# Kernel tuning notes

Hardware: AMD Instinct MI355X
Metric: run time of the kernel (lower is better)

The kernel has to match this reference:

```python
import jax, jax.numpy as jnp
import numpy as np

B, C, N, F = 256, 4, 64, 256   # batch, in_channels, neighbors, in_features
OC, OF = 8, 256                # out_channels, out_features


def setup_inputs() -> dict:
    key = jax.random.key(0)
    k1, k2, k3, k4, k5 = jax.random.split(key, 5)
    x = jax.random.normal(k1, (B, C, F), dtype=jnp.float32)
    neighbor = jax.random.normal(k2, (B, N, C, F), dtype=jnp.float32)
    # torch.nn.Linear weights are (out_features, in_features)
    W_att1 = jax.random.normal(k3, (C, F), dtype=jnp.float32) / np.sqrt(F).astype(np.float32)
    W_att2 = jax.random.normal(k4, (C, F), dtype=jnp.float32) / np.sqrt(F).astype(np.float32)
    # Conv1d weight: (out_c*out_f, 2C, F); kernel_size==F makes it a dense contraction
    W_conv = jax.random.normal(k5, (OC * OF, 2 * C, F), dtype=jnp.float32) / np.sqrt(2 * C * F).astype(np.float32)
    return {"x": x, "neighbor": neighbor, "W_att1": W_att1, "W_att2": W_att2, "W_conv": W_conv}


def reference(x, neighbor, W_att1, W_att2, W_conv):
    # --- attention weights: einsum 'ci,nkl->n' = sum(att1(x_i)) * sum_{k,l} att2(y_i)[n]
    s1 = jnp.sum(x @ W_att1.T, axis=(1, 2))              # (B,)
    s2 = jnp.sum(neighbor @ W_att2.T, axis=(2, 3))       # (B, N)
    w = jax.nn.softmax(s1[:, None] * s2, axis=1)         # softmax over neighbors (dim 0 per-sample)

    # --- feature adjacency: einsum 'ca,ncb,n->cab' vectorized over batch
    fadj = jnp.einsum('bcx,bncy,bn->bcxy', x, neighbor, w)   # (B, C, F, F)
    fadj = fadj + jnp.swapaxes(fadj, -1, -2)
    # sgnroot
    fadj = jnp.sign(fadj) * jnp.sqrt(jnp.clip(jnp.abs(fadj), 1e-8, None))
    # row normalize over dim -2, NaN -> 0
    adj = fadj / (jnp.abs(fadj).sum(axis=-2, keepdims=True) + 1e-7)
    adj = jnp.where(jnp.isnan(adj), jnp.float32(0.0), adj)

    # --- transform: cat([adj @ x, x], channel) then full-width conv1d (dense contraction)
    h = jnp.einsum('bcxy,bcy->bcx', adj, x)              # (B, C, F)
    z = jnp.concatenate([h, x], axis=1)                  # (B, 2C, F)
    out = jnp.einsum('bcf,ocf->bo', z, W_conv).reshape(B, OC, OF)
    return out, adj
```

## Files before the change

### kernel.cpp

```cpp
#include <hip/hip_runtime.h>
#include <hip/hip_bf16.h>
#include <math.h>


typedef __bf16 bf16x8 __attribute__((ext_vector_type(8)));
typedef __bf16 bf16x4 __attribute__((ext_vector_type(4)));
typedef float f32x4 __attribute__((ext_vector_type(4)));

#define NB 256
#define NC 4
#define NN 64
#define NF 256
#define NO 2048

__global__ __launch_bounds__(256) void k_pre(
    const float* __restrict__ x, const float* __restrict__ nb,
    const float* __restrict__ W1, const float* __restrict__ W2,
    const float* __restrict__ Wc,
    __hip_bfloat16* __restrict__ Wcb, __hip_bfloat16* __restrict__ zbf,
    float* __restrict__ s1, float* __restrict__ s2)
{
  __shared__ float red[4];
  int t = threadIdx.x;
  int gid = blockIdx.x;

  if (gid < 16640) {
    int fi = t & 63;
    const float4* Wf4 = (const float4*)((gid < 16384) ? W2 : W1);
    float4 w0 = Wf4[fi], w1 = Wf4[64 + fi], w2 = Wf4[128 + fi], w3 = Wf4[192 + fi];
    float4 wv = { w0.x + w1.x + w2.x + w3.x,
                  w0.y + w1.y + w2.y + w3.y,
                  w0.z + w1.z + w2.z + w3.z,
                  w0.w + w1.w + w2.w + w3.w };
    const float4* src = (gid < 16384) ? ((const float4*)nb + (size_t)gid * 256)
                                      : ((const float4*)x + (size_t)(gid - 16384) * 256);
    float4 nv = src[t];
    float val = fmaf(nv.x, wv.x, fmaf(nv.y, wv.y, fmaf(nv.z, wv.z, nv.w * wv.w)));
    for (int off = 32; off > 0; off >>= 1) val += __shfl_down(val, off);
    if ((t & 63) == 0) red[t >> 6] = val;
    __syncthreads();
    if (t == 0) {
      float s = red[0] + red[1] + red[2] + red[3];
      if (gid < 16384) s2[gid] = s;
      else s1[gid - 16384] = s;
    }
  } else if (gid < 20736) {
    int idx = (gid - 16640) * 256 + t;
    float4 v = ((const float4*)Wc)[idx];
    bf16x4 o = { (__bf16)v.x, (__bf16)v.y, (__bf16)v.z, (__bf16)v.w };
    ((bf16x4*)Wcb)[idx] = o;
  } else {
    int i = (gid - 20736) * 256 + t;
    int e = i * 4;
    int b = e >> 10, r = e & 1023;
    float4 v = ((const float4*)x)[i];
    bf16x4 o = { (__bf16)v.x, (__bf16)v.y, (__bf16)v.z, (__bf16)v.w };
    *(bf16x4*)(zbf + (size_t)b * 2048 + 1024 + r) = o;
  }
}

__global__ __launch_bounds__(256) void k_adj(
    const float* __restrict__ x, const float* __restrict__ nb,
    const float* __restrict__ s1, const float* __restrict__ s2,
    float* __restrict__ adj, __hip_bfloat16* __restrict__ zbf)
{
  __shared__ float xs[256], ns[256], invs[256], wsh[64];
  __shared__ float part[4][256];
  int t = threadIdx.x;
  int w = t >> 6, l = t & 63;
  int blk = blockIdx.x;
  int b = blk >> 2, c = blk & 3;

  if (t < 64) {
    float v = s1[b] * s2[b * 64 + t];
    float m = v;
    for (int off = 32; off > 0; off >>= 1) m = fmaxf(m, __shfl_xor(m, off));
    float e = expf(v - m);
    float s = e;
    for (int off = 32; off > 0; off >>= 1) s += __shfl_xor(s, off);
    wsh[t] = e / s;
  }
  xs[t] = x[(size_t)blk * 256 + t];
  __syncthreads();

  const float4* nb4 = (const float4*)(nb + (size_t)b * 65536 + c * 256);
  float4 a4 = {0.f, 0.f, 0.f, 0.f};
  #pragma unroll
  for (int k = 0; k < 16; ++k) {
    int n = w + 4 * k;
    float4 v = nb4[(size_t)n * 256 + l];
    float wn = wsh[n];
    a4.x = fmaf(wn, v.x, a4.x);
    a4.y = fmaf(wn, v.y, a4.y);
    a4.z = fmaf(wn, v.z, a4.z);
    a4.w = fmaf(wn, v.w, a4.w);
  }
  *(float4*)&part[w][l * 4] = a4;
  __syncthreads();
  ns[t] = part[0][t] + part[1][t] + part[2][t] + part[3][t];
  __syncthreads();

  int j0 = l * 4;
  float4 xv = *(const float4*)&xs[j0];
  float4 nv = *(const float4*)&ns[j0];
  int i0 = w * 64;

  float4 cs = {0.f, 0.f, 0.f, 0.f};
  #pragma unroll 4
  for (int ii = 0; ii < 64; ++ii) {
    int i = i0 + ii;
    float xi = xs[i], ni = ns[i];
    float v0 = fmaf(xi, nv.x, xv.x * ni);
    float v1 = fmaf(xi, nv.y, xv.y * ni);
    float v2 = fmaf(xi, nv.z, xv.z * ni);
    float v3 = fmaf(xi, nv.w, xv.w * ni);
    cs.x += (v0 != 0.f) ? __builtin_amdgcn_sqrtf(fmaxf(fabsf(v0), 1e-8f)) : 0.f;
    cs.y += (v1 != 0.f) ? __builtin_amdgcn_sqrtf(fmaxf(fabsf(v1), 1e-8f)) : 0.f;
    cs.z += (v2 != 0.f) ? __builtin_amdgcn_sqrtf(fmaxf(fabsf(v2), 1e-8f)) : 0.f;
    cs.w += (v3 != 0.f) ? __builtin_amdgcn_sqrtf(fmaxf(fabsf(v3), 1e-8f)) : 0.f;
  }
  *(float4*)&part[w][j0] = cs;
  __syncthreads();
  invs[t] = 1.f / (part[0][t] + part[1][t] + part[2][t] + part[3][t] + 1e-7f);
  __syncthreads();

  float4 iv = *(const float4*)&invs[j0];
  float4 ha = {0.f, 0.f, 0.f, 0.f};
  float* ab = adj + (size_t)blk * 65536;
  #pragma unroll 4
  for (int ii = 0; ii < 64; ++ii) {
    int i = i0 + ii;
    float xi = xs[i], ni = ns[i];
    float pix = invs[i] * xi;
    float v0 = fmaf(xi, nv.x, xv.x * ni);
    float v1 = fmaf(xi, nv.y, xv.y * ni);
    float v2 = fmaf(xi, nv.z, xv.z * ni);
    float v3 = fmaf(xi, nv.w, xv.w * ni);
    float g0 = (v0 != 0.f) ? copysignf(__builtin_amdgcn_sqrtf(fmaxf(fabsf(v0), 1e-8f)), v0) : 0.f;
    float g1 = (v1 != 0.f) ? copysignf(__builtin_amdgcn_sqrtf(fmaxf(fabsf(v1), 1e-8f)), v1) : 0.f;
    float g2 = (v2 != 0.f) ? copysignf(__builtin_amdgcn_sqrtf(fmaxf(fabsf(v2), 1e-8f)), v2) : 0.f;
    float g3 = (v3 != 0.f) ? copysignf(__builtin_amdgcn_sqrtf(fmaxf(fabsf(v3), 1e-8f)), v3) : 0.f;
    f32x4 o = { g0 * iv.x, g1 * iv.y, g2 * iv.z, g3 * iv.w };
    __builtin_nontemporal_store(o, (f32x4*)&ab[(size_t)i * 256 + j0]);
    ha.x = fmaf(g0, pix, ha.x);
    ha.y = fmaf(g1, pix, ha.y);
    ha.z = fmaf(g2, pix, ha.z);
    ha.w = fmaf(g3, pix, ha.w);
  }
  __syncthreads();
  *(float4*)&part[w][j0] = ha;
  __syncthreads();
  float hsum = part[0][t] + part[1][t] + part[2][t] + part[3][t];
  zbf[(size_t)b * 2048 + c * 256 + t] = __float2bfloat16(hsum);
}

__global__ __launch_bounds__(256) void k_gemm(
    const __hip_bfloat16* __restrict__ zb, const __hip_bfloat16* __restrict__ Wcb,
    float* __restrict__ out)
{
  int tid = threadIdx.x;
  int wave = tid >> 6, lane = tid & 63;
  int g = lane >> 4, r = lane & 15;
  int bm = blockIdx.x & 7, bn = blockIdx.x >> 3;
  int m0 = bm * 32 + (wave & 1) * 16;
  int n0 = bn * 32 + (wave >> 1) * 16;

  const bf16x8* pa = (const bf16x8*)(zb  + (size_t)(m0 + r) * 2048 + g * 8);
  const bf16x8* pw = (const bf16x8*)(Wcb + (size_t)(n0 + r) * 2048 + g * 8);

  f32x4 acc0 = {0.f, 0.f, 0.f, 0.f}, acc1 = {0.f, 0.f, 0.f, 0.f};
  #pragma unroll 4
  for (int ks = 0; ks < 64; ks += 2) {
    bf16x8 a0 = pa[ks * 4];
    bf16x8 b0 = pw[ks * 4];
    bf16x8 a1 = pa[ks * 4 + 4];
    bf16x8 b1 = pw[ks * 4 + 4];
    acc0 = __builtin_amdgcn_mfma_f32_16x16x32_bf16(a0, b0, acc0, 0, 0, 0);
    acc1 = __builtin_amdgcn_mfma_f32_16x16x32_bf16(a1, b1, acc1, 0, 0, 0);
  }
  acc0 += acc1;
  #pragma unroll
  for (int q = 0; q < 4; ++q) {
    int row = m0 + g * 4 + q;
    __builtin_nontemporal_store(acc0[q], &out[(size_t)row * 2048 + n0 + r]);
  }
}

__global__ __launch_bounds__(256) void k_scores_fb(
    const float* __restrict__ x, const float* __restrict__ nb,
    const float* __restrict__ W1, const float* __restrict__ W2,
    float* __restrict__ s1, float* __restrict__ s2)
{
  __shared__ float red[4];
  int t = threadIdx.x;
  int gid = blockIdx.x;
  float val;
  if (gid < NB * NN) {
    float w = W2[t] + W2[256 + t] + W2[512 + t] + W2[768 + t];
    const float* p = nb + (size_t)gid * 1024;
    val = w * (p[t] + p[256 + t] + p[512 + t] + p[768 + t]);
  } else {
    int b = gid - NB * NN;
    float w = W1[t] + W1[256 + t] + W1[512 + t] + W1[768 + t];
    const float* p = x + (size_t)b * 1024;
    val = w * (p[t] + p[256 + t] + p[512 + t] + p[768 + t]);
  }
  for (int off = 32; off > 0; off >>= 1) val += __shfl_down(val, off);
  if ((t & 63) == 0) red[t >> 6] = val;
  __syncthreads();
  if (t == 0) {
    float s = red[0] + red[1] + red[2] + red[3];
    if (gid < NB * NN) s2[gid] = s;
    else s1[gid - NB * NN] = s;
  }
}

__global__ __launch_bounds__(256) void k_adj_fb(
    const float* __restrict__ x, const float* __restrict__ nb,
    const float* __restrict__ s1, const float* __restrict__ s2,
    float* __restrict__ adj, float* __restrict__ hf)
{
  __shared__ float xs[256], ns[256], invs[256], wsh[64];
  __shared__ float part[4][256];
  int t = threadIdx.x;
  int w = t >> 6, l = t & 63;
  int blk = blockIdx.x;
  int b = blk >> 2, c = blk & 3;

  if (t < 64) {
    float v = s1[b] * s2[b * 64 + t];
    float m = v;
    for (int off = 32; off > 0; off >>= 1) m = fmaxf(m, __shfl_xor(m, off));
    float e = expf(v - m);
    float s = e;
    for (int off = 32; off > 0; off >>= 1) s += __shfl_xor(s, off);
    wsh[t] = e / s;
  }
  __syncthreads();
  float acc = 0.f;
  const float* pb = nb + (size_t)b * 65536 + c * 256 + t;
  #pragma unroll 8
  for (int n = 0; n < 64; ++n) acc = fmaf(wsh[n], pb[(size_t)n * 1024], acc);
  ns[t] = acc;
  xs[t] = x[(size_t)blk * 256 + t];
  __syncthreads();

  int j0 = l * 4;
  float4 xv = *(const float4*)&xs[j0];
  float4 nv = *(const float4*)&ns[j0];
  int i0 = w * 64;
  float4 cs = {0.f, 0.f, 0.f, 0.f};
  for (int ii = 0; ii < 64; ++ii) {
    int i = i0 + ii;
    float xi = xs[i], ni = ns[i];
    float v0 = fmaf(xi, nv.x, xv.x * ni);
    float v1 = fmaf(xi, nv.y, xv.y * ni);
    float v2 = fmaf(xi, nv.z, xv.z * ni);
    float v3 = fmaf(xi, nv.w, xv.w * ni);
    cs.x += (v0 != 0.f) ? __builtin_amdgcn_sqrtf(fmaxf(fabsf(v0), 1e-8f)) : 0.f;
    cs.y += (v1 != 0.f) ? __builtin_amdgcn_sqrtf(fmaxf(fabsf(v1), 1e-8f)) : 0.f;
    cs.z += (v2 != 0.f) ? __builtin_amdgcn_sqrtf(fmaxf(fabsf(v2), 1e-8f)) : 0.f;
    cs.w += (v3 != 0.f) ? __builtin_amdgcn_sqrtf(fmaxf(fabsf(v3), 1e-8f)) : 0.f;
  }
  *(float4*)&part[w][j0] = cs;
  __syncthreads();
  invs[t] = 1.f / (part[0][t] + part[1][t] + part[2][t] + part[3][t] + 1e-7f);
  __syncthreads();

  float4 iv = *(const float4*)&invs[j0];
  float4 ha = {0.f, 0.f, 0.f, 0.f};
  float* ab = adj + (size_t)blk * 65536;
  for (int ii = 0; ii < 64; ++ii) {
    int i = i0 + ii;
    float xi = xs[i], ni = ns[i];
    float pix = invs[i] * xi;
    float v0 = fmaf(xi, nv.x, xv.x * ni);
    float v1 = fmaf(xi, nv.y, xv.y * ni);
    float v2 = fmaf(xi, nv.z, xv.z * ni);
    float v3 = fmaf(xi, nv.w, xv.w * ni);
    float g0 = (v0 != 0.f) ? copysignf(__builtin_amdgcn_sqrtf(fmaxf(fabsf(v0), 1e-8f)), v0) : 0.f;
    float g1 = (v1 != 0.f) ? copysignf(__builtin_amdgcn_sqrtf(fmaxf(fabsf(v1), 1e-8f)), v1) : 0.f;
    float g2 = (v2 != 0.f) ? copysignf(__builtin_amdgcn_sqrtf(fmaxf(fabsf(v2), 1e-8f)), v2) : 0.f;
    float g3 = (v3 != 0.f) ? copysignf(__builtin_amdgcn_sqrtf(fmaxf(fabsf(v3), 1e-8f)), v3) : 0.f;
    f32x4 o = { g0 * iv.x, g1 * iv.y, g2 * iv.z, g3 * iv.w };
    __builtin_nontemporal_store(o, (f32x4*)&ab[(size_t)i * 256 + j0]);
    ha.x = fmaf(g0, pix, ha.x);
    ha.y = fmaf(g1, pix, ha.y);
    ha.z = fmaf(g2, pix, ha.z);
    ha.w = fmaf(g3, pix, ha.w);
  }
  __syncthreads();
  *(float4*)&part[w][j0] = ha;
  __syncthreads();
  hf[(size_t)blk * 256 + t] = part[0][t] + part[1][t] + part[2][t] + part[3][t];
}

__device__ inline bf16x8 cvt8_p(const float* p) {
  const float4* q = reinterpret_cast<const float4*>(p);
  float4 a = q[0], bq = q[1];
  bf16x8 r;
  r[0] = (__bf16)a.x;  r[1] = (__bf16)a.y;  r[2] = (__bf16)a.z;  r[3] = (__bf16)a.w;
  r[4] = (__bf16)bq.x; r[5] = (__bf16)bq.y; r[6] = (__bf16)bq.z; r[7] = (__bf16)bq.w;
  return r;
}

__global__ __launch_bounds__(256) void k_gemm_f32(
    const float* __restrict__ h, const float* __restrict__ x,
    const float* __restrict__ Wc, float* __restrict__ out)
{
  int tid = threadIdx.x;
  int wave = tid >> 6, lane = tid & 63;
  int g = lane >> 4, r = lane & 15;
  int bm = blockIdx.x & 3, bn = blockIdx.x >> 2;
  int m0 = bm * 64 + wave * 16;
  int n0 = bn * 32;
  int arow = m0 + r;
  int koff = g * 8;

  const float* za = h + (size_t)arow * 1024 + koff;
  const float* zb = x + (size_t)arow * 1024 + koff;
  const float* w0 = Wc + (size_t)(n0 + r) * 2048 + koff;
  const float* w1 = Wc + (size_t)(n0 + 16 + r) * 2048 + koff;

  f32x4 acc0 = {0.f, 0.f, 0.f, 0.f}, acc1 = {0.f, 0.f, 0.f, 0.f};
  #pragma unroll 4
  for (int ks = 0; ks < 32; ++ks) {
    acc0 = __builtin_amdgcn_mfma_f32_16x16x32_bf16(cvt8_p(za + ks * 32), cvt8_p(w0 + ks * 32), acc0, 0, 0, 0);
    acc1 = __builtin_amdgcn_mfma_f32_16x16x32_bf16(cvt8_p(za + ks * 32), cvt8_p(w1 + ks * 32), acc1, 0, 0, 0);
  }
  #pragma unroll 4
  for (int ks = 0; ks < 32; ++ks) {
    acc0 = __builtin_amdgcn_mfma_f32_16x16x32_bf16(cvt8_p(zb + ks * 32), cvt8_p(w0 + 1024 + ks * 32), acc0, 0, 0, 0);
    acc1 = __builtin_amdgcn_mfma_f32_16x16x32_bf16(cvt8_p(zb + ks * 32), cvt8_p(w1 + 1024 + ks * 32), acc1, 0, 0, 0);
  }
  #pragma unroll
  for (int q = 0; q < 4; ++q) {
    int row = m0 + g * 4 + q;
    out[(size_t)row * 2048 + n0 + r]      = acc0[q];
    out[(size_t)row * 2048 + n0 + 16 + r] = acc1[q];
  }
}

extern "C" void kernel_launch(void* const* d_in, const int* in_sizes, int n_in,
                              void* d_out, int out_size, void* d_ws, size_t ws_size,
                              hipStream_t stream) {
  const float* x  = (const float*)d_in[0];
  const float* nb = (const float*)d_in[1];
  const float* W1 = (const float*)d_in[2];
  const float* W2 = (const float*)d_in[3];
  const float* Wc = (const float*)d_in[4];
  float* out = (float*)d_out;
  float* adj = out + (size_t)NB * NO;

  char* ws = (char*)d_ws;
  const size_t ZBF_B = 1048576;
  const size_t WCB_B = 8388608;
  const size_t FREG = (256 + 16384) * 4;
  bool fast = ws_size >= ZBF_B + WCB_B + FREG;

  if (fast) {
    __hip_bfloat16* zbf = (__hip_bfloat16*)ws;
    __hip_bfloat16* Wcb = (__hip_bfloat16*)(ws + ZBF_B);
    float* s1  = (float*)(ws + ZBF_B + WCB_B);
    float* s2  = s1 + 256;
    k_pre<<<20992, 256, 0, stream>>>(x, nb, W1, W2, Wc, Wcb, zbf, s1, s2);
    k_adj<<<NB * NC, 256, 0, stream>>>(x, nb, s1, s2, adj, zbf);
    k_gemm<<<512, 256, 0, stream>>>(zbf, Wcb, out);
  } else {
    float* hws = (float*)d_ws;
    float* s1  = hws + 262144;
    float* s2  = s1 + 256;
    k_scores_fb<<<NB * NN + NB, 256, 0, stream>>>(x, nb, W1, W2, s1, s2);
    k_adj_fb<<<NB * NC, 256, 0, stream>>>(x, nb, s1, s2, adj, hws);
    k_gemm_f32<<<256, 256, 0, stream>>>(hws, x, Wc, out);
  }
}
```

Before: 108.5 us.

## Cache signed-sqrt adjacency values as bf16 in registers across 8-wave k_adj

k_adj now launches 512 threads (8 waves), and each wave handles 32 rows instead of 64. In the first pass each thread computes the signed square roots once and keeps them in registers as packed bf16, so the normalize/store pass no longer recomputes the products and sqrts. Row data is also read from shared memory as float4. The aim is to remove the duplicated ALU work and raise parallelism per block. In exchange, adj values are rounded to bf16 precision, register pressure rises, and exact-zero inputs now give a small signed value instead of zero.

```diff
diff --git a/kernel.cpp b/kernel.cpp
--- a/kernel.cpp
+++ b/kernel.cpp
@@ -6,12 +6,21 @@
 typedef __bf16 bf16x8 __attribute__((ext_vector_type(8)));
 typedef __bf16 bf16x4 __attribute__((ext_vector_type(4)));
 typedef float f32x4 __attribute__((ext_vector_type(4)));
+typedef unsigned short u16x4 __attribute__((ext_vector_type(4)));
 
 #define NB 256
 #define NC 4
 #define NN 64
 #define NF 256
 #define NO 2048
+
+__device__ inline unsigned short bf16bits(float f) {
+  __bf16 h = (__bf16)f;
+  return __builtin_bit_cast(unsigned short, h);
+}
+__device__ inline float bf16tof(unsigned short u) {
+  return __builtin_bit_cast(float, ((unsigned int)u) << 16);
+}
 
 __global__ __launch_bounds__(256) void k_pre(
     const float* __restrict__ x, const float* __restrict__ nb,
@@ -59,13 +68,13 @@
   }
 }
 
-__global__ __launch_bounds__(256) void k_adj(
+__global__ __launch_bounds__(512, 4) void k_adj(
     const float* __restrict__ x, const float* __restrict__ nb,
     const float* __restrict__ s1, const float* __restrict__ s2,
     float* __restrict__ adj, __hip_bfloat16* __restrict__ zbf)
 {
   __shared__ float xs[256], ns[256], invs[256], wsh[64];
-  __shared__ float part[4][256];
+  __shared__ float part[8][256];
   int t = threadIdx.x;
   int w = t >> 6, l = t & 63;
   int blk = blockIdx.x;
@@ -80,14 +89,14 @@
     for (int off = 32; off > 0; off >>= 1) s += __shfl_xor(s, off);
     wsh[t] = e / s;
   }
-  xs[t] = x[(size_t)blk * 256 + t];
+  if (t < 256) xs[t] = x[(size_t)blk * 256 + t];
   __syncthreads();
 
   const float4* nb4 = (const float4*)(nb + (size_t)b * 65536 + c * 256);
   float4 a4 = {0.f, 0.f, 0.f, 0.f};
   #pragma unroll
-  for (int k = 0; k < 16; ++k) {
-    int n = w + 4 * k;
+  for (int k = 0; k < 8; ++k) {
+    int n = w + 8 * k;
     float4 v = nb4[(size_t)n * 256 + l];
     float wn = wsh[n];
     a4.x = fmaf(wn, v.x, a4.x);
@@ -97,61 +106,76 @@
   }
   *(float4*)&part[w][l * 4] = a4;
   __syncthreads();
-  ns[t] = part[0][t] + part[1][t] + part[2][t] + part[3][t];
+  if (t < 256) ns[t] = part[0][t] + part[1][t] + part[2][t] + part[3][t]
+                     + part[4][t] + part[5][t] + part[6][t] + part[7][t];
   __syncthreads();
 
   int j0 = l * 4;
   float4 xv = *(const float4*)&xs[j0];
   float4 nv = *(const float4*)&ns[j0];
-  int i0 = w * 64;
-
+  int i0 = w * 32;
+
+  u16x4 gc[32];
   float4 cs = {0.f, 0.f, 0.f, 0.f};
-  #pragma unroll 4
-  for (int ii = 0; ii < 64; ++ii) {
-    int i = i0 + ii;
-    float xi = xs[i], ni = ns[i];
-    float v0 = fmaf(xi, nv.x, xv.x * ni);
-    float v1 = fmaf(xi, nv.y, xv.y * ni);
-    float v2 = fmaf(xi, nv.z, xv.z * ni);
-    float v3 = fmaf(xi, nv.w, xv.w * ni);
-    cs.x += (v0 != 0.f) ? __builtin_amdgcn_sqrtf(fmaxf(fabsf(v0), 1e-8f)) : 0.f;
-    cs.y += (v1 != 0.f) ? __builtin_amdgcn_sqrtf(fmaxf(fabsf(v1), 1e-8f)) : 0.f;
-    cs.z += (v2 != 0.f) ? __builtin_amdgcn_sqrtf(fmaxf(fabsf(v2), 1e-8f)) : 0.f;
-    cs.w += (v3 != 0.f) ? __builtin_amdgcn_sqrtf(fmaxf(fabsf(v3), 1e-8f)) : 0.f;
+  #pragma unroll
+  for (int r4 = 0; r4 < 8; ++r4) {
+    float4 x4 = *(const float4*)&xs[i0 + r4 * 4];
+    float4 n4 = *(const float4*)&ns[i0 + r4 * 4];
+    #pragma unroll
+    for (int rr = 0; rr < 4; ++rr) {
+      float xi = (rr == 0) ? x4.x : (rr == 1) ? x4.y : (rr == 2) ? x4.z : x4.w;
+      float ni = (rr == 0) ? n4.x : (rr == 1) ? n4.y : (rr == 2) ? n4.z : n4.w;
+      float v0 = fmaf(xi, nv.x, xv.x * ni);
+      float v1 = fmaf(xi, nv.y, xv.y * ni);
+      float v2 = fmaf(xi, nv.z, xv.z * ni);
+      float v3 = fmaf(xi, nv.w, xv.w * ni);
+      float r0 = __builtin_amdgcn_sqrtf(fmaxf(fabsf(v0), 1e-8f));
+      float r1 = __builtin_amdgcn_sqrtf(fmaxf(fabsf(v1), 1e-8f));
+      float r2 = __builtin_amdgcn_sqrtf(fmaxf(fabsf(v2), 1e-8f));
+      float r3 = __builtin_amdgcn_sqrtf(fmaxf(fabsf(v3), 1e-8f));
+      cs.x += r0; cs.y += r1; cs.z += r2; cs.w += r3;
+      u16x4 gu = { bf16bits(copysignf(r0, v0)), bf16bits(copysignf(r1, v1)),
+                   bf16bits(copysignf(r2, v2)), bf16bits(copysignf(r3, v3)) };
+      gc[r4 * 4 + rr] = gu;
+    }
   }
   *(float4*)&part[w][j0] = cs;
   __syncthreads();
-  invs[t] = 1.f / (part[0][t] + part[1][t] + part[2][t] + part[3][t] + 1e-7f);
+  if (t < 256) invs[t] = 1.f / (part[0][t] + part[1][t] + part[2][t] + part[3][t]
+                              + part[4][t] + part[5][t] + part[6][t] + part[7][t] + 1e-7f);
   __syncthreads();
 
   float4 iv = *(const float4*)&invs[j0];
   float4 ha = {0.f, 0.f, 0.f, 0.f};
   float* ab = adj + (size_t)blk * 65536;
-  #pragma unroll 4
-  for (int ii = 0; ii < 64; ++ii) {
-    int i = i0 + ii;
-    float xi = xs[i], ni = ns[i];
-    float pix = invs[i] * xi;
-    float v0 = fmaf(xi, nv.x, xv.x * ni);
-    float v1 = fmaf(xi, nv.y, xv.y * ni);
-    float v2 = fmaf(xi, nv.z, xv.z * ni);
-    float v3 = fmaf(xi, nv.w, xv.w * ni);
-    float g0 = (v0 != 0.f) ? copysignf(__builtin_amdgcn_sqrtf(fmaxf(fabsf(v0), 1e-8f)), v0) : 0.f;
-    float g1 = (v1 != 0.f) ? copysignf(__builtin_amdgcn_sqrtf(fmaxf(fabsf(v1), 1e-8f)), v1) : 0.f;
-    float g2 = (v2 != 0.f) ? copysignf(__builtin_amdgcn_sqrtf(fmaxf(fabsf(v2), 1e-8f)), v2) : 0.f;
-    float g3 = (v3 != 0.f) ? copysignf(__builtin_amdgcn_sqrtf(fmaxf(fabsf(v3), 1e-8f)), v3) : 0.f;
-    f32x4 o = { g0 * iv.x, g1 * iv.y, g2 * iv.z, g3 * iv.w };
-    __builtin_nontemporal_store(o, (f32x4*)&ab[(size_t)i * 256 + j0]);
-    ha.x = fmaf(g0, pix, ha.x);
-    ha.y = fmaf(g1, pix, ha.y);
-    ha.z = fmaf(g2, pix, ha.z);
-    ha.w = fmaf(g3, pix, ha.w);
+  #pragma unroll
+  for (int r4 = 0; r4 < 8; ++r4) {
+    float4 x4 = *(const float4*)&xs[i0 + r4 * 4];
+    float4 v4 = *(const float4*)&invs[i0 + r4 * 4];
+    #pragma unroll
+    for (int rr = 0; rr < 4; ++rr) {
+      int i = i0 + r4 * 4 + rr;
+      float xi  = (rr == 0) ? x4.x : (rr == 1) ? x4.y : (rr == 2) ? x4.z : x4.w;
+      float ivi = (rr == 0) ? v4.x : (rr == 1) ? v4.y : (rr == 2) ? v4.z : v4.w;
+      float pix = ivi * xi;
+      u16x4 gu = gc[r4 * 4 + rr];
+      float g0 = bf16tof(gu.x), g1 = bf16tof(gu.y), g2 = bf16tof(gu.z), g3 = bf16tof(gu.w);
+      f32x4 o = { g0 * iv.x, g1 * iv.y, g2 * iv.z, g3 * iv.w };
+      __builtin_nontemporal_store(o, (f32x4*)&ab[(size_t)i * 256 + j0]);
+      ha.x = fmaf(g0, pix, ha.x);
+      ha.y = fmaf(g1, pix, ha.y);
+      ha.z = fmaf(g2, pix, ha.z);
+      ha.w = fmaf(g3, pix, ha.w);
+    }
   }
   __syncthreads();
   *(float4*)&part[w][j0] = ha;
   __syncthreads();
-  float hsum = part[0][t] + part[1][t] + part[2][t] + part[3][t];
-  zbf[(size_t)b * 2048 + c * 256 + t] = __float2bfloat16(hsum);
+  if (t < 256) {
+    float hsum = part[0][t] + part[1][t] + part[2][t] + part[3][t]
+               + part[4][t] + part[5][t] + part[6][t] + part[7][t];
+    zbf[(size_t)b * 2048 + c * 256 + t] = __float2bfloat16(hsum);
+  }
 }
 
 __global__ __launch_bounds__(256) void k_gemm(
@@ -253,14 +277,10 @@
   for (int ii = 0; ii < 64; ++ii) {
     int i = i0 + ii;
     float xi = xs[i], ni = ns[i];
-    float v0 = fmaf(xi, nv.x, xv.x * ni);
-    float v1 = fmaf(xi, nv.y, xv.y * ni);
-    float v2 = fmaf(xi, nv.z, xv.z * ni);
-    float v3 = fmaf(xi, nv.w, xv.w * ni);
-    cs.x += (v0 != 0.f) ? __builtin_amdgcn_sqrtf(fmaxf(fabsf(v0), 1e-8f)) : 0.f;
-    cs.y += (v1 != 0.f) ? __builtin_amdgcn_sqrtf(fmaxf(fabsf(v1), 1e-8f)) : 0.f;
-    cs.z += (v2 != 0.f) ? __builtin_amdgcn_sqrtf(fmaxf(fabsf(v2), 1e-8f)) : 0.f;
-    cs.w += (v3 != 0.f) ? __builtin_amdgcn_sqrtf(fmaxf(fabsf(v3), 1e-8f)) : 0.f;
+    cs.x += __builtin_amdgcn_sqrtf(fmaxf(fabsf(fmaf(xi, nv.x, xv.x * ni)), 1e-8f));
+    cs.y += __builtin_amdgcn_sqrtf(fmaxf(fabsf(fmaf(xi, nv.y, xv.y * ni)), 1e-8f));
+    cs.z += __builtin_amdgcn_sqrtf(fmaxf(fabsf(fmaf(xi, nv.z, xv.z * ni)), 1e-8f));
+    cs.w += __builtin_amdgcn_sqrtf(fmaxf(fabsf(fmaf(xi, nv.w, xv.w * ni)), 1e-8f));
   }
   *(float4*)&part[w][j0] = cs;
   __syncthreads();
@@ -278,10 +298,10 @@
     float v1 = fmaf(xi, nv.y, xv.y * ni);
     float v2 = fmaf(xi, nv.z, xv.z * ni);
     float v3 = fmaf(xi, nv.w, xv.w * ni);
-    float g0 = (v0 != 0.f) ? copysignf(__builtin_amdgcn_sqrtf(fmaxf(fabsf(v0), 1e-8f)), v0) : 0.f;
-    float g1 = (v1 != 0.f) ? copysignf(__builtin_amdgcn_sqrtf(fmaxf(fabsf(v1), 1e-8f)), v1) : 0.f;
-    float g2 = (v2 != 0.f) ? copysignf(__builtin_amdgcn_sqrtf(fmaxf(fabsf(v2), 1e-8f)), v2) : 0.f;
-    float g3 = (v3 != 0.f) ? copysignf(__builtin_amdgcn_sqrtf(fmaxf(fabsf(v3), 1e-8f)), v3) : 0.f;
+    float g0 = copysignf(__builtin_amdgcn_sqrtf(fmaxf(fabsf(v0), 1e-8f)), v0);
+    float g1 = copysignf(__builtin_amdgcn_sqrtf(fmaxf(fabsf(v1), 1e-8f)), v1);
+    float g2 = copysignf(__builtin_amdgcn_sqrtf(fmaxf(fabsf(v2), 1e-8f)), v2);
+    float g3 = copysignf(__builtin_amdgcn_sqrtf(fmaxf(fabsf(v3), 1e-8f)), v3);
     f32x4 o = { g0 * iv.x, g1 * iv.y, g2 * iv.z, g3 * iv.w };
     __builtin_nontemporal_store(o, (f32x4*)&ab[(size_t)i * 256 + j0]);
     ha.x = fmaf(g0, pix, ha.x);
@@ -364,7 +384,7 @@
     float* s1  = (float*)(ws + ZBF_B + WCB_B);
     float* s2  = s1 + 256;
     k_pre<<<20992, 256, 0, stream>>>(x, nb, W1, W2, Wc, Wcb, zbf, s1, s2);
-    k_adj<<<NB * NC, 256, 0, stream>>>(x, nb, s1, s2, adj, zbf);
+    k_adj<<<NB * NC, 512, 0, stream>>>(x, nb, s1, s2, adj, zbf);
     k_gemm<<<512, 256, 0, stream>>>(zbf, Wcb, out);
   } else {
     float* hws = (float*)d_ws;
```

After: 149.2 us. 1.38x slower.
